# Performance work log

Hardware: AMD Instinct MI355X
Metric: run time of the kernel (lower is better)

## Reference

```python
import jax, jax.numpy as jnp
import numpy as np

EMB, HEADS, DEPTH, SEQ, BATCH = 256, 8, 4, 8192, 4
DH = EMB // HEADS  # 32
FF = 4 * EMB
EPS = 1e-5


def setup_inputs() -> dict:
    key = jax.random.key(0)
    ks = jax.random.split(key, 8)
    w = lambda k, shape: jax.random.normal(k, shape, dtype=jnp.float32) * 0.02
    D = DEPTH
    return {
        "x": jax.random.normal(ks[0], (BATCH, SEQ, EMB), dtype=jnp.float32),
        "Wq": w(ks[1], (D, EMB, EMB)),
        "Wk": w(ks[2], (D, EMB, EMB)),
        "Wv": w(ks[3], (D, EMB, EMB)),
        "Wo": w(ks[4], (D, EMB, EMB)),
        "bo": jnp.zeros((D, EMB), jnp.float32),
        "ln1_g": jnp.ones((D, EMB), jnp.float32),
        "ln1_b": jnp.zeros((D, EMB), jnp.float32),
        "W1": w(ks[5], (D, EMB, FF)),
        "b1": jnp.zeros((D, FF), jnp.float32),
        "W2": w(ks[6], (D, FF, EMB)),
        "b2": jnp.zeros((D, EMB), jnp.float32),
        "ln2_g": jnp.ones((D, EMB), jnp.float32),
        "ln2_b": jnp.zeros((D, EMB), jnp.float32),
    }


def _layernorm(x, g, b):
    mu = x.mean(-1, keepdims=True)
    var = ((x - mu) ** 2).mean(-1, keepdims=True)
    return (x - mu) * jax.lax.rsqrt(var + EPS) * g + b


def _linear_attn(x, Wq, Wk, Wv, Wo, bo):
    # lucidrains linear_attn: q,k scaled by d**-0.25; softmax q over feature dim,
    # k over sequence dim; context = k^T v (per head), out = q @ context.
    b, n, dm = x.shape
    split = lambda t: t.reshape(b, n, HEADS, DH).transpose(0, 2, 1, 3)  # -> bhnd
    scale = DH ** -0.25
    q = jax.nn.softmax(split(x @ Wq) * scale, axis=-1)   # over d
    k = jax.nn.softmax(split(x @ Wk) * scale, axis=-2)   # over n
    v = split(x @ Wv)
    context = jnp.einsum('bhnd,bhne->bhde', k, v)        # [b,h,d,d]
    out = jnp.einsum('bhnd,bhde->bhne', q, context)      # [b,h,n,d]
    out = out.transpose(0, 2, 1, 3).reshape(b, n, dm)
    return out @ Wo + bo


def _forward(x, Wq, Wk, Wv, Wo, bo, ln1_g, ln1_b, W1, b1, W2, b2, ln2_g, ln2_b):
    for i in range(DEPTH):
        h = _layernorm(x, ln1_g[i], ln1_b[i])
        x = x + _linear_attn(h, Wq[i], Wk[i], Wv[i], Wo[i], bo[i])
        h = _layernorm(x, ln2_g[i], ln2_b[i])
        x = x + (jax.nn.gelu(h @ W1[i] + b1[i], approximate=False) @ W2[i] + b2[i])
    return x


def reference(x, Wq, Wk, Wv, Wo, bo, ln1_g, ln1_b, W1, b1, W2, b2, ln2_g, ln2_b):
    return _forward(x, Wq, Wk, Wv, Wo, bo, ln1_g, ln1_b, W1, b1, W2, b2, ln2_g, ln2_b)
```

## Files before the change

kernel.cpp:

```cpp
#include <hip/hip_runtime.h>
#include <hip/hip_bf16.h>

typedef __attribute__((ext_vector_type(8))) short bf16x8;
typedef __attribute__((ext_vector_type(4))) float f32x4;

#define EMB 256
#define HEADS 8
#define DH 32
#define SEQ 8192
#define BATCH 4
#define NROWS (SEQ*BATCH)
#define FFD 1024
#define DEPTH 4
#define QKVN 768
#define SCALE 0.42044820762685725f
#define NCHUNK 128
#define ROWS_PER_CHUNK (SEQ/NCHUNK)

static __device__ __forceinline__ float bf2f(ushort u){
  union { unsigned int i; float f; } x; x.i = ((unsigned int)u) << 16; return x.f;
}
static __device__ __forceinline__ ushort f2bf(float f){
  union { __hip_bfloat16 h; ushort u; } cv;
  cv.h = __float2bfloat16(f);
  return cv.u;
}
static __device__ __forceinline__ float gelu_f(float v){
  float y = 0.7978845608028654f * (v + 0.044715f*v*v*v);
  float e = __expf(2.0f*y);
  return 0.5f*v*(1.0f + (1.0f - 2.0f/(e + 1.0f)));
}

static __device__ __forceinline__ void gload_lds16(const ushort* g, ushort* l){
  __builtin_amdgcn_global_load_lds(
      (const __attribute__((address_space(1))) unsigned int*)(uintptr_t)g,
      (__attribute__((address_space(3))) unsigned int*)(uintptr_t)l,
      16, 0, 0);
}

__global__ __launch_bounds__(256) void prep_weights(
    const float* __restrict__ Wq, const float* __restrict__ Wk,
    const float* __restrict__ Wv, const float* __restrict__ Wo,
    const float* __restrict__ W1, const float* __restrict__ W2,
    ushort* __restrict__ wqkv_t, ushort* __restrict__ wo_t,
    ushort* __restrict__ w1_t, ushort* __restrict__ w2_t)
{
  __shared__ float tile[32][33];
  int bid = blockIdx.x;
  int L = bid / 768, r = bid % 768;
  const float* src; ushort* dst; int K, N, tidx;
  if (r < 192){ int which = r >> 6; tidx = r & 63;
    src = (which==0?Wq:which==1?Wk:Wv) + (long)L*65536;
    dst = wqkv_t + (long)L*QKVN*EMB + which*EMB*EMB; K=256; N=256;
  } else if (r < 256){ tidx = r-192; src = Wo + (long)L*65536; dst = wo_t + (long)L*65536; K=256; N=256; }
  else if (r < 512){ tidx = r-256; src = W1 + (long)L*262144; dst = w1_t + (long)L*262144; K=256; N=1024; }
  else { tidx = r-512; src = W2 + (long)L*262144; dst = w2_t + (long)L*262144; K=1024; N=256; }
  int tn = N >> 5;
  int tk = tidx / tn, tj = tidx % tn;
  int k0 = tk*32, n0 = tj*32;
  int c = threadIdx.x & 31, r0 = threadIdx.x >> 5;
  #pragma unroll
  for (int i=0;i<4;i++){
    int rr = r0 + i*8;
    tile[rr][c] = src[(long)(k0+rr)*N + n0 + c];
  }
  __syncthreads();
  #pragma unroll
  for (int i=0;i<4;i++){
    int rr = r0 + i*8;
    dst[(long)(n0+rr)*K + k0 + c] = f2bf(tile[c][rr]);
  }
}

__global__ __launch_bounds__(256) void ln_kernel(const float* __restrict__ x,
    const float* __restrict__ g, const float* __restrict__ bb,
    ushort* __restrict__ h)
{
  int wid = threadIdx.x >> 6, lane = threadIdx.x & 63;
  long row = (long)blockIdx.x*4 + wid;
  const float4 xv = *(const float4*)(x + row*EMB + lane*4);
  float s = xv.x+xv.y+xv.z+xv.w;
  float s2 = xv.x*xv.x+xv.y*xv.y+xv.z*xv.z+xv.w*xv.w;
  #pragma unroll
  for (int m=1;m<64;m<<=1){ s += __shfl_xor(s,m,64); s2 += __shfl_xor(s2,m,64); }
  float mean = s * (1.0f/EMB);
  float inv = rsqrtf(s2*(1.0f/EMB) - mean*mean + 1e-5f);
  float4 gv = *(const float4*)(g + lane*4);
  float4 bv = *(const float4*)(bb + lane*4);
  ushort4 o;
  o.x = f2bf((xv.x-mean)*inv*gv.x + bv.x);
  o.y = f2bf((xv.y-mean)*inv*gv.y + bv.y);
  o.z = f2bf((xv.z-mean)*inv*gv.z + bv.z);
  o.w = f2bf((xv.w-mean)*inv*gv.w + bv.w);
  *(ushort4*)(h + row*EMB + lane*4) = o;
}

template<int MODE, int BM, int BN, int BK, int GSWAP>
__global__ __launch_bounds__(512, 2) void gemm_bt(
    const ushort* __restrict__ A, const ushort* __restrict__ Bt,
    int M, int N, int K,
    const float* __restrict__ bias,
    const float* __restrict__ xinf, const ushort* __restrict__ xinb,
    float* __restrict__ xoutf, ushort* __restrict__ xoutb,
    ushort* __restrict__ outb,
    const float* __restrict__ lng, const float* __restrict__ lnb)
{
  constexpr int NF = BN/64;
  constexpr int MR = BM/32;
  constexpr int MH = MR/4;
  constexpr int KK = BK/32;
  constexpr int CPR = BK/8;
  constexpr int AI = BM*BK/4096;
  constexpr int BI = BN*BK/4096;
  constexpr int TI = AI + BI;
  constexpr int NPH = KK*MH;
  __shared__ ushort LDSraw[2*BM*BK + 2*BN*BK];
  ushort* Abuf0 = LDSraw;
  ushort* Abuf1 = LDSraw + BM*BK;
  ushort* Bbuf0 = LDSraw + 2*BM*BK;
  ushort* Bbuf1 = LDSraw + 2*BM*BK + BN*BK;
  int t = threadIdx.x;
  int lane = t & 63, wid = t >> 6;
  int wr = wid >> 2, wc = wid & 3;
  int wrb = wr*(BM/2), wcb = wc*(BN/4);
  long rowA0, colB0;
  if (GSWAP){ rowA0 = (long)blockIdx.y * BM; colB0 = (long)blockIdx.x * BN; }
  else      { rowA0 = (long)blockIdx.x * BM; colB0 = (long)blockIdx.y * BN; }
  const ushort* gA[AI]; int dA[AI];
  #pragma unroll
  for (int i=0;i<AI;i++){
    int l = i*512 + t;
    int row = l / CPR;
    int clog = (t % CPR) ^ (row & (CPR-1));
    gA[i] = A + (rowA0 + row)*(long)K + clog*8;
    dA[i] = l*8;
  }
  const ushort* gB[BI]; int dB[BI];
  #pragma unroll
  for (int i=0;i<BI;i++){
    int l = i*512 + t;
    int row = l / CPR;
    int clog = (t % CPR) ^ (row & (CPR-1));
    gB[i] = Bt + (colB0 + row)*(long)K + clog*8;
    dB[i] = l*8;
  }
  ushort* Ac = Abuf0; ushort* An = Abuf1;
  ushort* Bc = Bbuf0; ushort* Bn = Bbuf1;
  f32x4 acc[MR][NF] = {};
  int fr = lane & 15, cr4 = lane >> 4;
  int nsteps = K / BK;
  #pragma unroll
  for (int i=0;i<AI;i++) gload_lds16(gA[i], Ac + dA[i]);
  #pragma unroll
  for (int i=0;i<BI;i++) gload_lds16(gB[i], Bc + dB[i]);
  asm volatile("s_waitcnt vmcnt(0)" ::: "memory");
  __syncthreads();
  for (int s = 0; s < nsteps; ++s){
    bool pf = (s+1 < nsteps);
    long knext = (long)(s+1) * BK;
    #pragma unroll
    for (int kk=0; kk<KK; ++kk){
      int chunk = (((kk*4 + cr4)) ^ (fr & (CPR-1))) << 3;
      bf16x8 bv[NF];
      #pragma unroll
      for (int n=0;n<NF;n++)
        bv[n] = *(const bf16x8*)(Bc + (wcb + n*16 + fr)*BK + chunk);
      #pragma unroll
      for (int mh=0; mh<MH; ++mh){
        int sp = kk*MH + mh;
        bf16x8 av[4];
        #pragma unroll
        for (int m=0;m<4;m++)
          av[m] = *(const bf16x8*)(Ac + (wrb + (mh*4+m)*16 + fr)*BK + chunk);
        if (pf){
          #pragma unroll
          for (int j=0;j<TI;j++){
            if (j*NPH >= sp*TI && j*NPH < (sp+1)*TI){
              if (j < AI) gload_lds16(gA[j]+knext, An+dA[j]);
              else        gload_lds16(gB[j-AI]+knext, Bn+dB[j-AI]);
            }
          }
        }
        __builtin_amdgcn_s_setprio(1);
        #pragma unroll
        for (int m=0;m<4;m++){
          #pragma unroll
          for (int n=0;n<NF;n++)
            acc[mh*4+m][n] = __builtin_amdgcn_mfma_f32_16x16x32_bf16(av[m], bv[n], acc[mh*4+m][n], 0,0,0);
        }
        __builtin_amdgcn_s_setprio(0);
      }
    }
    asm volatile("s_waitcnt vmcnt(0)" ::: "memory");
    __syncthreads();
    ushort* tp;
    tp = Ac; Ac = An; An = tp;
    tp = Bc; Bc = Bn; Bn = tp;
  }
  constexpr int BNP = BN + 4;
  constexpr int ROUNDS = BM/32;
  constexpr int RPH = BM/64;
  float* bounce = (float*)LDSraw;
  int fq = lane >> 4;
  constexpr int TPR = BN/4;
  int rdrow = t / TPR;
  int rdcol = (t % TPR) * 4;
  constexpr int RPP = 512 / TPR;
  constexpr int PASSES = 32 / RPP;
  long gcf = colB0 + rdcol;
  float4 bv4e = {0,0,0,0}, g4e = {0,0,0,0}, b4e = {0,0,0,0};
  if (MODE==2 || MODE==3 || MODE==4) bv4e = *(const float4*)&bias[gcf];
  if (MODE==3 || MODE==4){ g4e = *(const float4*)&lng[gcf]; b4e = *(const float4*)&lnb[gcf]; }
  #pragma unroll
  for (int r = 0; r < ROUNDS; ++r){
    __syncthreads();
    if (wr == r / RPH){
      int mb = (r % RPH)*2;
      #pragma unroll
      for (int m4=0;m4<2;m4++){
        #pragma unroll
        for (int n=0;n<NF;n++){
          #pragma unroll
          for (int i=0;i<4;i++)
            bounce[(m4*16 + fq*4 + i)*BNP + wcb + n*16 + fr] = acc[mb+m4][n][i];
        }
      }
    }
    __syncthreads();
    long gr0 = rowA0 + r*32;
    #pragma unroll
    for (int p=0;p<PASSES;p++){
      int lr = p*RPP + rdrow;
      long gr = gr0 + lr;
      float4 v = *(float4*)&bounce[lr*BNP + rdcol];
      if (MODE==0){
        ushort4 o; o.x=f2bf(v.x); o.y=f2bf(v.y); o.z=f2bf(v.z); o.w=f2bf(v.w);
        *(ushort4*)&outb[gr*N + gcf] = o;
      } else if (MODE==2){
        ushort4 o;
        o.x = f2bf(gelu_f(v.x + bv4e.x)); o.y = f2bf(gelu_f(v.y + bv4e.y));
        o.z = f2bf(gelu_f(v.z + bv4e.z)); o.w = f2bf(gelu_f(v.w + bv4e.w));
        *(ushort4*)&outb[gr*N + gcf] = o;
      } else {
        float xo0, xo1, xo2, xo3;
        if (MODE==3){
          const float4 xo = *(const float4*)&xinf[gr*N + gcf];
          xo0=xo.x; xo1=xo.y; xo2=xo.z; xo3=xo.w;
        } else {
          const ushort4 xb = *(const ushort4*)&xinb[gr*N + gcf];
          xo0=bf2f(xb.x); xo1=bf2f(xb.y); xo2=bf2f(xb.z); xo3=bf2f(xb.w);
        }
        v.x += bv4e.x + xo0; v.y += bv4e.y + xo1;
        v.z += bv4e.z + xo2; v.w += bv4e.w + xo3;
        ushort4 xw;
        xw.x=f2bf(v.x); xw.y=f2bf(v.y); xw.z=f2bf(v.z); xw.w=f2bf(v.w);
        *(ushort4*)&xoutb[gr*N + gcf] = xw;
        float s1 = v.x+v.y+v.z+v.w;
        float s2 = v.x*v.x+v.y*v.y+v.z*v.z+v.w*v.w;
        #pragma unroll
        for (int mm=1;mm<64;mm<<=1){ s1 += __shfl_xor(s1,mm,64); s2 += __shfl_xor(s2,mm,64); }
        float mean = s1 * (1.0f/EMB);
        float inv = rsqrtf(s2*(1.0f/EMB) - mean*mean + 1e-5f);
        ushort4 o;
        o.x = f2bf((v.x-mean)*inv*g4e.x + b4e.x);
        o.y = f2bf((v.y-mean)*inv*g4e.y + b4e.y);
        o.z = f2bf((v.z-mean)*inv*g4e.z + b4e.z);
        o.w = f2bf((v.w-mean)*inv*g4e.w + b4e.w);
        *(ushort4*)&outb[gr*EMB + gcf] = o;
      }
    }
  }
}

template<int MODE>
__global__ __launch_bounds__(512) void ff_fused(
    const ushort* __restrict__ A, const ushort* __restrict__ w1t,
    const ushort* __restrict__ w2t,
    const float* __restrict__ b1, const float* __restrict__ b2,
    const ushort* __restrict__ xinb,
    float* __restrict__ xoutf, ushort* __restrict__ xoutb,
    ushort* __restrict__ hout,
    const float* __restrict__ lng, const float* __restrict__ lnb)
{
  __shared__ ushort As[128*256];
  __shared__ ushort W1b[64*256];
  __shared__ ushort W2b[256*64];
  __shared__ ushort Ps[128*68];
  int t = threadIdx.x, lane = t & 63, wid = t >> 6;
  int fr = lane & 15, cr4 = lane >> 4, fq = lane >> 4;
  long rowA0 = (long)blockIdx.x * 128;
  #pragma unroll
  for (int i=0;i<8;i++){
    int l = i*512 + t;
    int row = l >> 5;
    int clog = (l & 31) ^ (row & 31);
    gload_lds16(A + (rowA0+row)*256 + clog*8, As + l*8);
  }
  #pragma unroll
  for (int i=0;i<4;i++){
    int l = i*512 + t;
    int row = l >> 5;
    int clog = (l & 31) ^ (row & 31);
    gload_lds16(w1t + row*256 + clog*8, W1b + l*8);
  }
  asm volatile("s_waitcnt vmcnt(0)" ::: "memory");
  __syncthreads();
  int rwP = (wid & 3)*32, fwP = (wid >> 2)*32;
  int rw2 = (wid >> 2)*64, cw2 = (wid & 3)*64;
  f32x4 accC[4][4] = {};
  for (int j = 0; j < 16; ++j){
    float bvp0 = b1[j*64 + fwP + fr];
    float bvp1 = b1[j*64 + fwP + 16 + fr];
    f32x4 accP[2][2] = {};
    #pragma unroll
    for (int kk=0; kk<8; ++kk){
      if (kk < 4){
        int l = kk*512 + t;
        int row = l >> 3, c = l & 7;
        int clog = c ^ (row & 7);
        gload_lds16(w2t + row*1024 + j*64 + clog*8, W2b + l*8);
      }
      int ci = kk*4 + cr4;
      bf16x8 av[2], wv[2];
      #pragma unroll
      for (int m=0;m<2;m++){
        int row = rwP + m*16 + fr;
        av[m] = *(const bf16x8*)(As + row*256 + ((ci ^ (row&31)) << 3));
      }
      #pragma unroll
      for (int n=0;n<2;n++){
        int row = fwP + n*16 + fr;
        wv[n] = *(const bf16x8*)(W1b + row*256 + ((ci ^ (row&31)) << 3));
      }
      __builtin_amdgcn_s_setprio(1);
      #pragma unroll
      for (int m=0;m<2;m++){
        #pragma unroll
        for (int n=0;n<2;n++)
          accP[m][n] = __builtin_amdgcn_mfma_f32_16x16x32_bf16(av[m], wv[n], accP[m][n], 0,0,0);
      }
      __builtin_amdgcn_s_setprio(0);
    }
    #pragma unroll
    for (int n=0;n<2;n++){
      float bv = (n==0) ? bvp0 : bvp1;
      #pragma unroll
      for (int m=0;m<2;m++){
        #pragma unroll
        for (int i2=0;i2<4;i2++){
          int row = rwP + m*16 + fq*4 + i2;
          Ps[row*68 + fwP + n*16 + fr] = f2bf(gelu_f(accP[m][n][i2] + bv));
        }
      }
    }
    asm volatile("s_waitcnt vmcnt(0)" ::: "memory");
    __syncthreads();
    bool pw1 = (j+1 < 16);
    #pragma unroll
    for (int kk2=0; kk2<2; ++kk2){
      if (pw1 && kk2==0){
        #pragma unroll
        for (int ii=0;ii<4;ii++){
          int l = ii*512 + t;
          int row = l >> 5;
          int clog = (l & 31) ^ (row & 31);
          gload_lds16(w1t + (long)(j+1)*64*256 + row*256 + clog*8, W1b + l*8);
        }
      }
      int ci2 = kk2*4 + cr4;
      bf16x8 pv[4], wv2[4];
      #pragma unroll
      for (int m=0;m<4;m++){
        int row = rw2 + m*16 + fr;
        pv[m] = *(const bf16x8*)(Ps + row*68 + ci2*8);
      }
      #pragma unroll
      for (int n=0;n<4;n++){
        int row = cw2 + n*16 + fr;
        wv2[n] = *(const bf16x8*)(W2b + row*64 + ((ci2 ^ (row&7)) << 3));
      }
      __builtin_amdgcn_s_setprio(1);
      #pragma unroll
      for (int m=0;m<4;m++){
        #pragma unroll
        for (int n=0;n<4;n++)
          accC[m][n] = __builtin_amdgcn_mfma_f32_16x16x32_bf16(pv[m], wv2[n], accC[m][n], 0,0,0);
      }
      __builtin_amdgcn_s_setprio(0);
    }
    asm volatile("s_waitcnt vmcnt(0)" ::: "memory");
    __syncthreads();
  }
  float* bounce = (float*)As;
  int rdrow = t >> 6;
  int rdcol = (t & 63) * 4;
  const float4 bv4 = *(const float4*)&b2[rdcol];
  float4 g4 = {0,0,0,0}, b4 = {0,0,0,0};
  if (MODE==4){ g4 = *(const float4*)&lng[rdcol]; b4 = *(const float4*)&lnb[rdcol]; }
  #pragma unroll
  for (int r = 0; r < 4; ++r){
    __syncthreads();
    if ((wid >> 2) == (r >> 1)){
      int mb = (r & 1)*2;
      #pragma unroll
      for (int m4=0;m4<2;m4++){
        #pragma unroll
        for (int n=0;n<4;n++){
          #pragma unroll
          for (int i2=0;i2<4;i2++)
            bounce[(m4*16 + fq*4 + i2)*260 + cw2 + n*16 + fr] = accC[mb+m4][n][i2];
        }
      }
    }
    __syncthreads();
    long gr0 = rowA0 + r*32;
    #pragma unroll
    for (int p=0;p<4;p++){
      int lr = p*8 + rdrow;
      long gr = gr0 + lr;
      float4 v = *(float4*)&bounce[lr*260 + rdcol];
      const ushort4 xb4 = *(const ushort4*)&xinb[gr*EMB + rdcol];
      v.x += bv4.x + bf2f(xb4.x); v.y += bv4.y + bf2f(xb4.y);
      v.z += bv4.z + bf2f(xb4.z); v.w += bv4.w + bf2f(xb4.w);
      if (MODE==5){
        *(float4*)&xoutf[gr*EMB + rdcol] = v;
      } else {
        ushort4 xw;
        xw.x=f2bf(v.x); xw.y=f2bf(v.y); xw.z=f2bf(v.z); xw.w=f2bf(v.w);
        *(ushort4*)&xoutb[gr*EMB + rdcol] = xw;
        float s1 = v.x+v.y+v.z+v.w;
        float s2 = v.x*v.x+v.y*v.y+v.z*v.z+v.w*v.w;
        #pragma unroll
        for (int mm=1;mm<64;mm<<=1){ s1 += __shfl_xor(s1,mm,64); s2 += __shfl_xor(s2,mm,64); }
        float mean = s1 * (1.0f/EMB);
        float inv = rsqrtf(s2*(1.0f/EMB) - mean*mean + 1e-5f);
        ushort4 o;
        o.x = f2bf((v.x-mean)*inv*g4.x + b4.x);
        o.y = f2bf((v.y-mean)*inv*g4.y + b4.y);
        o.z = f2bf((v.z-mean)*inv*g4.z + b4.z);
        o.w = f2bf((v.w-mean)*inv*g4.w + b4.w);
        *(ushort4*)&hout[gr*EMB + rdcol] = o;
      }
    }
  }
}

__global__ __launch_bounds__(256) void colstats_partial(const ushort* __restrict__ qkv,
    float* __restrict__ pmax, float* __restrict__ psum)
{
  int ch = blockIdx.x, b = blockIdx.y;
  int t = threadIdx.x;
  const ushort* base = qkv + ((long)b*SEQ + (long)ch*ROWS_PER_CHUNK)*QKVN + EMB + t;
  float m[4] = {-1e30f,-1e30f,-1e30f,-1e30f};
  float s[4] = {0.f,0.f,0.f,0.f};
  #pragma unroll 2
  for (int n = 0; n < ROWS_PER_CHUNK; n += 4){
    #pragma unroll
    for (int j=0;j<4;j++){
      float v = bf2f(base[(long)(n+j)*QKVN]) * SCALE;
      float m2 = fmaxf(m[j], v);
      s[j] = s[j]*__expf(m[j]-m2) + __expf(v-m2);
      m[j] = m2;
    }
  }
  float M = fmaxf(fmaxf(m[0],m[1]), fmaxf(m[2],m[3]));
  float S = s[0]*__expf(m[0]-M) + s[1]*__expf(m[1]-M)
          + s[2]*__expf(m[2]-M) + s[3]*__expf(m[3]-M);
  long idx = ((long)b*NCHUNK + ch)*EMB + t;
  pmax[idx] = M; psum[idx] = S;
}

__global__ __launch_bounds__(256) void colstats_reduce(const float* __restrict__ pmax,
    const float* __restrict__ psum, float* __restrict__ kmax, float* __restrict__ ksum)
{
  int b = blockIdx.x, t = threadIdx.x;
  const float* pm = pmax + (long)b*NCHUNK*EMB + t;
  const float* ps = psum + (long)b*NCHUNK*EMB + t;
  float m = -1e30f, s = 0.f;
  for (int c = 0; c < NCHUNK; ++c){
    float cm = pm[(long)c*EMB], cs = ps[(long)c*EMB];
    float m2 = fmaxf(m, cm);
    s = s*__expf(m-m2) + cs*__expf(cm-m2);
    m = m2;
  }
  kmax[b*EMB + t] = m;
  ksum[b*EMB + t] = s;
}

__global__ __launch_bounds__(256) void ctx_partial(
    const ushort* __restrict__ qkv, const float* __restrict__ kmax,
    float* __restrict__ ctx_part)
{
  constexpr int LT = 72;
  __shared__ ushort ekT[32*LT];
  __shared__ ushort vvT[32*LT];
  int ch = blockIdx.x, h = blockIdx.y, b = blockIdx.z;
  int t = threadIdx.x, lane = t & 63, wid = t >> 6;
  long nbase = (long)b*SEQ + ch*512;
  int lrow = t >> 2, lseg = (t & 3) << 3;
  float km[8];
  #pragma unroll
  for (int j=0;j<8;j++) km[j] = kmax[b*256 + h*DH + lseg + j];
  int wstep = wid & 1, wdr = (wid >> 1) << 4;
  f32x4 acc0 = {}, acc1 = {};
  int frow = lane & 15, g8 = (lane >> 4) << 3;
  for (int st = 0; st < 8; ++st){
    long n0 = nbase + st*64;
    const ushort* gk = qkv + (n0 + lrow)*QKVN + EMB + h*DH + lseg;
    uint4 kv = *(const uint4*)gk;
    uint4 vv = *(const uint4*)(gk + EMB);
    __syncthreads();
    const ushort* kp = (const ushort*)&kv;
    const ushort* vp = (const ushort*)&vv;
    #pragma unroll
    for (int j=0;j<8;j++){
      float f = bf2f(kp[j])*SCALE;
      ekT[(lseg+j)*LT + lrow] = f2bf(__expf(f - km[j]));
      vvT[(lseg+j)*LT + lrow] = vp[j];
    }
    __syncthreads();
    bf16x8 afr = *(const bf16x8*)(ekT + (wdr + frow)*LT + wstep*32 + g8);
    bf16x8 bf0 = *(const bf16x8*)(vvT + frow*LT + wstep*32 + g8);
    bf16x8 bf1 = *(const bf16x8*)(vvT + (16 + frow)*LT + wstep*32 + g8);
    acc0 = __builtin_amdgcn_mfma_f32_16x16x32_bf16(afr, bf0, acc0, 0,0,0);
    acc1 = __builtin_amdgcn_mfma_f32_16x16x32_bf16(afr, bf1, acc1, 0,0,0);
  }
  int fq = lane >> 4;
  long pb = (((long)(b*HEADS+h))*32 + (ch*2+wstep))*1024;
  #pragma unroll
  for (int i=0;i<4;i++){
    ctx_part[pb + (wdr + fq*4 + i)*32 + frow] = acc0[i];
    ctx_part[pb + (wdr + fq*4 + i)*32 + 16 + frow] = acc1[i];
  }
}

__global__ __launch_bounds__(256) void ctx_reduce(const float* __restrict__ ctx_part,
    const float* __restrict__ ksum, ushort* __restrict__ ctxT)
{
  int bh = blockIdx.x; int b = bh >> 3, h = bh & 7;
  int t = threadIdx.x; int d = t >> 3, e4 = (t & 7) << 2;
  const float* p = ctx_part + (long)bh*32768 + d*32 + e4;
  float sx=0, sy=0, sz=0, sw=0;
  for (int c=0;c<32;c++){
    const float4 v = *(const float4*)(p + c*1024);
    sx+=v.x; sy+=v.y; sz+=v.z; sw+=v.w;
  }
  float inv = 1.0f / ksum[b*256 + h*DH + d];
  long base = (long)bh*1024;
  ctxT[base + (e4+0)*32 + d] = f2bf(sx*inv);
  ctxT[base + (e4+1)*32 + d] = f2bf(sy*inv);
  ctxT[base + (e4+2)*32 + d] = f2bf(sz*inv);
  ctxT[base + (e4+3)*32 + d] = f2bf(sw*inv);
}

__global__ __launch_bounds__(256) void attn_out(
    const ushort* __restrict__ qkv, const ushort* __restrict__ ctxT,
    ushort* __restrict__ ao)
{
  __shared__ ushort sq[4][16][264];
  int t = threadIdx.x, lane = t & 63, wid = t >> 6;
  long row0 = (long)blockIdx.x*64 + wid*16;
  int b = (int)(row0 / SEQ);
  int fr = lane & 15, g = lane >> 4;
  bf16x8 cf[8][2];
  #pragma unroll
  for (int h=0;h<8;h++){
    #pragma unroll
    for (int eh=0;eh<2;eh++)
      cf[h][eh] = *(const bf16x8*)(ctxT + ((long)(b*8+h)*32 + eh*16 + fr)*32 + g*8);
  }
  long gr = row0 + fr;
  #pragma unroll
  for (int hh=0;hh<2;hh++){
    int h = g*2 + hh;
    const ushort* qp = qkv + gr*QKVN + h*DH;
    union { uint4 v[4]; ushort u[32]; } qq;
    qq.v[0]=*(const uint4*)qp; qq.v[1]=*(const uint4*)(qp+8);
    qq.v[2]=*(const uint4*)(qp+16); qq.v[3]=*(const uint4*)(qp+24);
    float f[32]; float m = -1e30f;
    #pragma unroll
    for (int j=0;j<32;j++){ f[j] = bf2f(qq.u[j])*SCALE; m = fmaxf(m, f[j]); }
    float ssum = 0.f;
    #pragma unroll
    for (int j=0;j<32;j++){ f[j] = __expf(f[j]-m); ssum += f[j]; }
    float inv = 1.0f/ssum;
    union { uint4 v[4]; ushort u[32]; } oo;
    #pragma unroll
    for (int j=0;j<32;j++) oo.u[j] = f2bf(f[j]*inv);
    ushort* dst = &sq[wid][fr][h*DH];
    #pragma unroll
    for (int c2=0;c2<4;c2++) *(uint4*)(dst + c2*8) = oo.v[c2];
  }
  __syncthreads();
  #pragma unroll
  for (int h=0;h<8;h++){
    bf16x8 af = *(const bf16x8*)(&sq[wid][fr][h*DH + g*8]);
    f32x4 z = {};
    f32x4 o0 = __builtin_amdgcn_mfma_f32_16x16x32_bf16(af, cf[h][0], z, 0,0,0);
    f32x4 o1 = __builtin_amdgcn_mfma_f32_16x16x32_bf16(af, cf[h][1], z, 0,0,0);
    #pragma unroll
    for (int i=0;i<4;i++){
      long r = row0 + g*4 + i;
      ao[r*EMB + h*DH + fr]      = f2bf(o0[i]);
      ao[r*EMB + h*DH + 16 + fr] = f2bf(o1[i]);
    }
  }
}

extern "C" void kernel_launch(void* const* d_in, const int* in_sizes, int n_in,
                              void* d_out, int out_size, void* d_ws, size_t ws_size,
                              hipStream_t stream)
{
  const float* x_in = (const float*)d_in[0];
  const float* Wq  = (const float*)d_in[1];
  const float* Wk  = (const float*)d_in[2];
  const float* Wv  = (const float*)d_in[3];
  const float* Wo  = (const float*)d_in[4];
  const float* bo  = (const float*)d_in[5];
  const float* ln1g = (const float*)d_in[6];
  const float* ln1b = (const float*)d_in[7];
  const float* W1  = (const float*)d_in[8];
  const float* b1  = (const float*)d_in[9];
  const float* W2  = (const float*)d_in[10];
  const float* b2  = (const float*)d_in[11];
  const float* ln2g = (const float*)d_in[12];
  const float* ln2b = (const float*)d_in[13];
  float* xout = (float*)d_out;

  char* ws = (char*)d_ws;
  ushort* h_buf  = (ushort*)ws;  ws += (long)NROWS*EMB*2;
  ushort* xb     = (ushort*)ws;  ws += (long)NROWS*EMB*2;
  ushort* big    = (ushort*)ws;  ws += (long)NROWS*FFD*2;
  ushort* wqkv_t = (ushort*)ws;  ws += (long)DEPTH*QKVN*EMB*2;
  ushort* wo_t   = (ushort*)ws;  ws += (long)DEPTH*EMB*EMB*2;
  ushort* w1_t   = (ushort*)ws;  ws += (long)DEPTH*FFD*EMB*2;
  ushort* w2_t   = (ushort*)ws;  ws += (long)DEPTH*EMB*FFD*2;
  float*  kmax   = (float*)ws;   ws += (long)BATCH*EMB*4;
  float*  ksumv  = (float*)ws;   ws += (long)BATCH*EMB*4;
  float*  ctx_part = (float*)ws; ws += (long)BATCH*HEADS*32*1024*4;
  ushort* ctxT   = (ushort*)ws;  ws += (long)BATCH*HEADS*1024*2;
  float*  pmax   = (float*)ws;   ws += (long)BATCH*NCHUNK*EMB*4;
  float*  psum   = (float*)ws;   ws += (long)BATCH*NCHUNK*EMB*4;

  prep_weights<<<3072, 256, 0, stream>>>(Wq, Wk, Wv, Wo, W1, W2, wqkv_t, wo_t, w1_t, w2_t);
  ln_kernel<<<NROWS/4, 256, 0, stream>>>(x_in, ln1g, ln1b, h_buf);

  ushort* qkv = big;
  for (int L = 0; L < DEPTH; ++L){
    gemm_bt<0,128,128,64,1><<<dim3(QKVN/128, NROWS/128), 512, 0, stream>>>(
        h_buf, wqkv_t + (long)L*QKVN*EMB, NROWS, QKVN, EMB,
        nullptr, nullptr, nullptr, nullptr, nullptr, qkv, nullptr, nullptr);
    colstats_partial<<<dim3(NCHUNK, BATCH), 256, 0, stream>>>(qkv, pmax, psum);
    colstats_reduce<<<BATCH, 256, 0, stream>>>(pmax, psum, kmax, ksumv);
    ctx_partial<<<dim3(16, HEADS, BATCH), 256, 0, stream>>>(qkv, kmax, ctx_part);
    ctx_reduce<<<32, 256, 0, stream>>>(ctx_part, ksumv, ctxT);
    attn_out<<<NROWS/64, 256, 0, stream>>>(qkv, ctxT, h_buf);
    if (L == 0){
      gemm_bt<3,128,256,64,0><<<dim3(NROWS/128, 1), 512, 0, stream>>>(
          h_buf, wo_t, NROWS, EMB, EMB,
          bo, x_in, nullptr, nullptr, xb, h_buf, ln2g, ln2b);
    } else {
      gemm_bt<4,128,256,64,0><<<dim3(NROWS/128, 1), 512, 0, stream>>>(
          h_buf, wo_t + (long)L*EMB*EMB, NROWS, EMB, EMB,
          bo + L*EMB, nullptr, xb, nullptr, xb, h_buf,
          ln2g + L*EMB, ln2b + L*EMB);
    }
    if (L + 1 < DEPTH){
      ff_fused<4><<<256, 512, 0, stream>>>(
          h_buf, w1_t + (long)L*FFD*EMB, w2_t + (long)L*EMB*FFD,
          b1 + L*FFD, b2 + L*EMB, xb, nullptr, xb, h_buf,
          ln1g + (L+1)*EMB, ln1b + (L+1)*EMB);
    } else {
      ff_fused<5><<<256, 512, 0, stream>>>(
          h_buf, w1_t + (long)L*FFD*EMB, w2_t + (long)L*EMB*FFD,
          b1 + L*FFD, b2 + L*EMB, xb, xout, nullptr, nullptr,
          nullptr, nullptr);
    }
  }
}
```

Measured before the change: 582.5 us.

## Keep A tile in registers and double-buffer W1/W2 slices in LDS

```diff
diff --git a/kernel.cpp b/kernel.cpp
--- a/kernel.cpp
+++ b/kernel.cpp
@@ -282,62 +282,78 @@
     ushort* __restrict__ hout,
     const float* __restrict__ lng, const float* __restrict__ lnb)
 {
-  __shared__ ushort As[128*256];
-  __shared__ ushort W1b[64*256];
-  __shared__ ushort W2b[256*64];
-  __shared__ ushort Ps[128*68];
+  __shared__ ushort LDS[4*16384 + 128*68];
+  ushort* W1buf0 = LDS;
+  ushort* W1buf1 = LDS + 16384;
+  ushort* W2buf0 = LDS + 32768;
+  ushort* W2buf1 = LDS + 49152;
+  ushort* Ps     = LDS + 65536;
   int t = threadIdx.x, lane = t & 63, wid = t >> 6;
   int fr = lane & 15, cr4 = lane >> 4, fq = lane >> 4;
   long rowA0 = (long)blockIdx.x * 128;
-  #pragma unroll
-  for (int i=0;i<8;i++){
-    int l = i*512 + t;
-    int row = l >> 5;
-    int clog = (l & 31) ^ (row & 31);
-    gload_lds16(A + (rowA0+row)*256 + clog*8, As + l*8);
+  int rwP = (wid & 3)*32, fwP = (wid >> 2)*32;
+  int rw2 = (wid >> 2)*64, cw2 = (wid & 3)*64;
+  bf16x8 areg[2][8];
+  #pragma unroll
+  for (int m=0;m<2;m++){
+    #pragma unroll
+    for (int kk=0;kk<8;kk++)
+      areg[m][kk] = *(const bf16x8*)(A + (rowA0 + rwP + m*16 + fr)*256 + (kk*4+cr4)*8);
   }
   #pragma unroll
   for (int i=0;i<4;i++){
     int l = i*512 + t;
     int row = l >> 5;
     int clog = (l & 31) ^ (row & 31);
-    gload_lds16(w1t + row*256 + clog*8, W1b + l*8);
+    gload_lds16(w1t + row*256 + clog*8, W1buf0 + l*8);
+  }
+  #pragma unroll
+  for (int i=0;i<4;i++){
+    int l = i*512 + t;
+    int row = l >> 3;
+    int clog = (l & 7) ^ (row & 7);
+    gload_lds16(w2t + row*1024 + clog*8, W2buf0 + l*8);
   }
   asm volatile("s_waitcnt vmcnt(0)" ::: "memory");
   __syncthreads();
-  int rwP = (wid & 3)*32, fwP = (wid >> 2)*32;
-  int rw2 = (wid >> 2)*64, cw2 = (wid & 3)*64;
   f32x4 accC[4][4] = {};
   for (int j = 0; j < 16; ++j){
+    int cur = j & 1;
+    const ushort* W1c = cur ? W1buf1 : W1buf0;
+    const ushort* W2c = cur ? W2buf1 : W2buf0;
+    ushort* W1a = cur ? W1buf0 : W1buf1;
+    ushort* W2a = cur ? W2buf0 : W2buf1;
+    bool pf = (j+1 < 16);
     float bvp0 = b1[j*64 + fwP + fr];
     float bvp1 = b1[j*64 + fwP + 16 + fr];
     f32x4 accP[2][2] = {};
     #pragma unroll
     for (int kk=0; kk<8; ++kk){
-      if (kk < 4){
-        int l = kk*512 + t;
-        int row = l >> 3, c = l & 7;
-        int clog = c ^ (row & 7);
-        gload_lds16(w2t + row*1024 + j*64 + clog*8, W2b + l*8);
-      }
-      int ci = kk*4 + cr4;
-      bf16x8 av[2], wv[2];
-      #pragma unroll
-      for (int m=0;m<2;m++){
-        int row = rwP + m*16 + fr;
-        av[m] = *(const bf16x8*)(As + row*256 + ((ci ^ (row&31)) << 3));
-      }
+      if (pf){
+        if (kk < 4){
+          int l = kk*512 + t;
+          int row = l >> 5;
+          int clog = (l & 31) ^ (row & 31);
+          gload_lds16(w1t + (long)(j+1)*16384 + row*256 + clog*8, W1a + l*8);
+        } else {
+          int l = (kk-4)*512 + t;
+          int row = l >> 3;
+          int clog = (l & 7) ^ (row & 7);
+          gload_lds16(w2t + row*1024 + (j+1)*64 + clog*8, W2a + l*8);
+        }
+      }
+      bf16x8 wv[2];
       #pragma unroll
       for (int n=0;n<2;n++){
         int row = fwP + n*16 + fr;
-        wv[n] = *(const bf16x8*)(W1b + row*256 + ((ci ^ (row&31)) << 3));
+        wv[n] = *(const bf16x8*)(W1c + row*256 + (((kk*4+cr4) ^ (row&31)) << 3));
       }
       __builtin_amdgcn_s_setprio(1);
       #pragma unroll
       for (int m=0;m<2;m++){
         #pragma unroll
         for (int n=0;n<2;n++)
-          accP[m][n] = __builtin_amdgcn_mfma_f32_16x16x32_bf16(av[m], wv[n], accP[m][n], 0,0,0);
+          accP[m][n] = __builtin_amdgcn_mfma_f32_16x16x32_bf16(areg[m][kk], wv[n], accP[m][n], 0,0,0);
       }
       __builtin_amdgcn_s_setprio(0);
     }
@@ -353,20 +369,10 @@
         }
       }
     }
-    asm volatile("s_waitcnt vmcnt(0)" ::: "memory");
-    __syncthreads();
-    bool pw1 = (j+1 < 16);
+    asm volatile("s_waitcnt lgkmcnt(0)" ::: "memory");
+    __builtin_amdgcn_s_barrier();
     #pragma unroll
     for (int kk2=0; kk2<2; ++kk2){
-      if (pw1 && kk2==0){
-        #pragma unroll
-        for (int ii=0;ii<4;ii++){
-          int l = ii*512 + t;
-          int row = l >> 5;
-          int clog = (l & 31) ^ (row & 31);
-          gload_lds16(w1t + (long)(j+1)*64*256 + row*256 + clog*8, W1b + l*8);
-        }
-      }
       int ci2 = kk2*4 + cr4;
       bf16x8 pv[4], wv2[4];
       #pragma unroll
@@ -377,7 +383,7 @@
       #pragma unroll
       for (int n=0;n<4;n++){
         int row = cw2 + n*16 + fr;
-        wv2[n] = *(const bf16x8*)(W2b + row*64 + ((ci2 ^ (row&7)) << 3));
+        wv2[n] = *(const bf16x8*)(W2c + row*64 + ((ci2 ^ (row&7)) << 3));
       }
       __builtin_amdgcn_s_setprio(1);
       #pragma unroll
@@ -389,9 +395,9 @@
       __builtin_amdgcn_s_setprio(0);
     }
     asm volatile("s_waitcnt vmcnt(0)" ::: "memory");
-    __syncthreads();
-  }
-  float* bounce = (float*)As;
+    __builtin_amdgcn_s_barrier();
+  }
+  float* bounce = (float*)LDS;
   int rdrow = t >> 6;
   int rdcol = (t & 63) * 4;
   const float4 bv4 = *(const float4*)&b2[rdcol];
```

Measured after the change: 701.8 us. 1.2x slower.
